# Kernel optimization log

Hardware: AMD Instinct MI355X
Metric: run time of the kernel (lower is better)

The kernel has to match this reference:

```python
import jax, jax.numpy as jnp
import numpy as np

NUM_COMPONENTS = 8   # component ids 1..8 present; 0 = background (excluded, as in ids[ids>0])
SMOOTH = 1e-5


def setup_inputs() -> dict:
    key = jax.random.key(0)
    k1, k2, k3 = jax.random.split(key, 3)
    B, H, W, D = 2, 160, 160, 160
    y_pred = jax.random.normal(k1, (B, 2, H, W, D), dtype=jnp.float32)
    y = jax.random.randint(k2, (B, 1, H, W, D), 0, 2).astype(jnp.int64)
    components = jax.random.randint(k3, (B, H, W, D), 0, NUM_COMPONENTS + 1).astype(jnp.int64)
    return {"y_pred": y_pred, "y": y, "components": components}


def _soft_dice_loss(inter, psum, tsum):
    # metric(masked_pred, masked_true, mask) = 1 - 2*sum(p*t)/(sum(p)+sum(t)), smoothed
    return 1.0 - (2.0 * inter + SMOOTH) / (psum + tsum + SMOOTH)


def reference(y_pred, y, components):
    # activation: softmax over channel dim 1 (binary logits)
    probs = jax.nn.softmax(y_pred, axis=1)                       # [B,2,H,W,D]
    # one-hot encode int labels -> [B,2,H,W,D] float
    true = jax.nn.one_hot(y[:, 0], y_pred.shape[1], axis=1, dtype=probs.dtype)
    B = probs.shape[0]
    V = components.shape[1] * components.shape[2] * components.shape[3]
    comp = components.reshape(B, V)
    # per-voxel channel-summed quantities (mask-multiply then reduce == segment reduce)
    pp = (probs * true).sum(axis=1).reshape(B, V)                # sum_c p*t
    sp = probs.sum(axis=1).reshape(B, V)                         # sum_c p
    st = true.sum(axis=1).reshape(B, V)                          # sum_c t
    cnt = jnp.ones((B, V), dtype=probs.dtype)

    def seg(d):
        return jax.vmap(lambda dd, cc: jax.ops.segment_sum(dd, cc, num_segments=NUM_COMPONENTS + 1))(d, comp)

    inter, psum, tsum, counts = seg(pp), seg(sp), seg(st), seg(cnt)
    # drop background (component id 0), as torch loops only over ids > 0
    inter, psum, tsum, counts = inter[:, 1:], psum[:, 1:], tsum[:, 1:], counts[:, 1:]
    dice = _soft_dice_loss(inter, psum, tsum)                    # [B, K]
    present = (counts > 0).astype(dice.dtype)                    # only ids in torch.unique
    per_sample = (dice * present).sum(axis=1) / jnp.maximum(present.sum(axis=1), 1.0)
    return per_sample.mean()
```

## Files before the change

kernel.cpp:

```cpp
#include <hip/hip_runtime.h>

#define NB 2
#define NCK 8
#define NVAL (NCK * 2)
#define NBINS (NB * NVAL)
#define SMOOTHF 1e-5f

#define TROW 18

__global__ __launch_bounds__(256) void cc_accum(
        const float* __restrict__ y_pred,
        const int* __restrict__ y,
        const int* __restrict__ comp,
        float* __restrict__ partial,
        int V4, int BPB, int nblk) {
    __shared__ __align__(8) float sacc[256 * TROW + 16 * 16];
    float* redbuf = &sacc[256 * TROW];

    float2* mybins = (float2*)&sacc[threadIdx.x * TROW];
    #pragma unroll
    for (int i = 0; i < 9; ++i) mybins[i] = make_float2(0.0f, 0.0f);

    const int b   = (blockIdx.x >= BPB) ? 1 : 0;
    const int blk = blockIdx.x - b * BPB;
    const int stride = BPB * 256;

    const float* p0 = y_pred + (size_t)b * 2 * ((size_t)V4 * 4);
    const float* p1 = p0 + (size_t)V4 * 4;
    const int4* yq = (const int4*)y    + (size_t)b * V4;
    const int4* cq = (const int4*)comp + (size_t)b * V4;

    for (int v = blk * 256 + threadIdx.x; v < V4; v += stride) {
        const float4 a0 = ((const float4*)p0)[v];
        const float4 a1 = ((const float4*)p1)[v];
        const int4 t = yq[v];
        const int4 c = cq[v];

        {
            const float d = a0.x - a1.x;
            const float p = 1.0f / (1.0f + __expf(t.x ? d : -d));
            float2 s = mybins[c.x]; s.x += p; s.y += 1.0f; mybins[c.x] = s;
        }
        {
            const float d = a0.y - a1.y;
            const float p = 1.0f / (1.0f + __expf(t.y ? d : -d));
            float2 s = mybins[c.y]; s.x += p; s.y += 1.0f; mybins[c.y] = s;
        }
        {
            const float d = a0.z - a1.z;
            const float p = 1.0f / (1.0f + __expf(t.z ? d : -d));
            float2 s = mybins[c.z]; s.x += p; s.y += 1.0f; mybins[c.z] = s;
        }
        {
            const float d = a0.w - a1.w;
            const float p = 1.0f / (1.0f + __expf(t.w ? d : -d));
            float2 s = mybins[c.w]; s.x += p; s.y += 1.0f; mybins[c.w] = s;
        }
    }
    __syncthreads();

    {
        const int v = threadIdx.x & 15, g = threadIdx.x >> 4;
        const int off = ((v >> 1) + 1) * 2 + (v & 1);
        float s = 0.0f;
        #pragma unroll
        for (int k = 0; k < 16; ++k)
            s += sacc[(g * 16 + k) * TROW + off];
        redbuf[v * 16 + g] = s;
    }
    __syncthreads();
    if (threadIdx.x < NVAL) {
        float s = 0.0f;
        #pragma unroll
        for (int g = 0; g < 16; ++g) s += redbuf[threadIdx.x * 16 + g];
        partial[(size_t)(b * NVAL + threadIdx.x) * nblk + blockIdx.x] = s;
    }
}

__global__ __launch_bounds__(256) void cc_reduce(
        const float* __restrict__ partial, float* __restrict__ fin,
        int half, int nblk) {
    const int bin = blockIdx.x;
    const int b = (bin >= NVAL) ? 1 : 0;
    const int c0 = b * half;
    float s = 0.0f;
    for (int i = threadIdx.x; i < half; i += 256)
        s += partial[(size_t)bin * nblk + c0 + i];
    #pragma unroll
    for (int off = 32; off; off >>= 1) s += __shfl_xor(s, off);
    __shared__ float w4[4];
    if ((threadIdx.x & 63) == 0) w4[threadIdx.x >> 6] = s;
    __syncthreads();
    if (threadIdx.x == 0) fin[bin] = w4[0] + w4[1] + w4[2] + w4[3];
}

__global__ void cc_final(const float* __restrict__ fin, float* __restrict__ out) {
    float total = 0.0f;
    for (int b = 0; b < NB; ++b) {
        float dsum = 0.0f, pc = 0.0f;
        for (int j = 0; j < NCK; ++j) {
            const float inter = fin[b * NVAL + 2 * j];
            const float cnt   = fin[b * NVAL + 2 * j + 1];
            if (cnt > 0.0f) {
                dsum += 1.0f - (2.0f * inter + SMOOTHF) / (2.0f * cnt + SMOOTHF);
                pc += 1.0f;
            }
        }
        total += dsum / fmaxf(pc, 1.0f);
    }
    out[0] = total / (float)NB;
}

extern "C" void kernel_launch(void* const* d_in, const int* in_sizes, int n_in,
                              void* d_out, int out_size, void* d_ws, size_t ws_size,
                              hipStream_t stream) {
    const float* y_pred = (const float*)d_in[0];
    const int*   y      = (const int*)d_in[1];
    const int*   comp   = (const int*)d_in[2];
    float* out = (float*)d_out;
    float* ws  = (float*)d_ws;

    const int nvox = in_sizes[1];
    const int V    = nvox / NB;
    const int V4   = V / 4;

    int BPB = 1024;
    int cap_rows = (int)((ws_size / sizeof(float) - NBINS) / NBINS);
    if (2 * BPB > cap_rows) BPB = cap_rows / 2;
    if (BPB > V4) BPB = V4;
    if (BPB < 1) BPB = 1;
    const int nblk = 2 * BPB;

    float* fin = ws + (size_t)NBINS * nblk;

    cc_accum<<<dim3(nblk), dim3(256), 0, stream>>>(y_pred, y, comp, ws, V4, BPB, nblk);
    cc_reduce<<<dim3(NBINS), dim3(256), 0, stream>>>(ws, fin, BPB, nblk);
    cc_final<<<dim3(1), dim3(1), 0, stream>>>(fin, out);
}
```

Baseline: 31.18 us.

## Fuse reduce and final kernels into one block, pad shared rows for banks

Partials are now stored block-major (32 slots per block, zeros in the other batch's slots), so one 1024-thread block can sum them with float4 loads and compute the dice loss in the same kernel. This replaces two launches (cc_reduce and cc_final) with one. Shared-memory rows also get a 2-float pad on alternate half-groups of 16 threads to cut bank conflicts in the per-thread histograms. The trade-off is that a single block reads all partials serially and twice as many partial values are written.

```diff
diff --git a/kernel.cpp b/kernel.cpp
--- a/kernel.cpp
+++ b/kernel.cpp
@@ -3,21 +3,22 @@
 #define NB 2
 #define NCK 8
 #define NVAL (NCK * 2)
-#define NBINS (NB * NVAL)
+#define NSL 32
 #define SMOOTHF 1e-5f
 
 #define TROW 18
+#define RBASE(t) ((t) * TROW + ((((t) >> 4) & 1) << 1))
 
 __global__ __launch_bounds__(256) void cc_accum(
         const float* __restrict__ y_pred,
         const int* __restrict__ y,
         const int* __restrict__ comp,
         float* __restrict__ partial,
-        int V4, int BPB, int nblk) {
-    __shared__ __align__(8) float sacc[256 * TROW + 16 * 16];
-    float* redbuf = &sacc[256 * TROW];
+        int V4, int BPB) {
+    __shared__ __align__(8) float sacc[256 * TROW + 4 + 16 * 16];
+    float* redbuf = &sacc[256 * TROW + 4];
 
-    float2* mybins = (float2*)&sacc[threadIdx.x * TROW];
+    float2* mybins = (float2*)&sacc[RBASE(threadIdx.x)];
     #pragma unroll
     for (int i = 0; i < 9; ++i) mybins[i] = make_float2(0.0f, 0.0f);
 
@@ -60,55 +61,89 @@
     __syncthreads();
 
     {
-        const int v = threadIdx.x & 15, g = threadIdx.x >> 4;
-        const int off = ((v >> 1) + 1) * 2 + (v & 1);
+        const int vv = threadIdx.x & 15, g = threadIdx.x >> 4;
+        const int off = ((vv >> 1) + 1) * 2 + (vv & 1);
         float s = 0.0f;
         #pragma unroll
         for (int k = 0; k < 16; ++k)
-            s += sacc[(g * 16 + k) * TROW + off];
-        redbuf[v * 16 + g] = s;
+            s += sacc[RBASE(g * 16 + k) + off];
+        redbuf[vv * 16 + g] = s;
     }
     __syncthreads();
-    if (threadIdx.x < NVAL) {
+    if (threadIdx.x < NSL) {
+        const int j = threadIdx.x, jb = j >> 4, jv = j & 15;
         float s = 0.0f;
-        #pragma unroll
-        for (int g = 0; g < 16; ++g) s += redbuf[threadIdx.x * 16 + g];
-        partial[(size_t)(b * NVAL + threadIdx.x) * nblk + blockIdx.x] = s;
+        if (jb == b) {
+            #pragma unroll
+            for (int g = 0; g < 16; ++g) s += redbuf[jv * 16 + g];
+        }
+        partial[(size_t)blockIdx.x * NSL + j] = s;
     }
 }
 
-__global__ __launch_bounds__(256) void cc_reduce(
-        const float* __restrict__ partial, float* __restrict__ fin,
-        int half, int nblk) {
-    const int bin = blockIdx.x;
-    const int b = (bin >= NVAL) ? 1 : 0;
-    const int c0 = b * half;
-    float s = 0.0f;
-    for (int i = threadIdx.x; i < half; i += 256)
-        s += partial[(size_t)bin * nblk + c0 + i];
-    #pragma unroll
-    for (int off = 32; off; off >>= 1) s += __shfl_xor(s, off);
-    __shared__ float w4[4];
-    if ((threadIdx.x & 63) == 0) w4[threadIdx.x >> 6] = s;
+__global__ __launch_bounds__(1024) void cc_finish(
+        const float* __restrict__ partial, float* __restrict__ out, int nblk) {
+    const int tid = threadIdx.x;
+    const float4* p4 = (const float4*)partial;
+    const int nf = nblk * (NSL / 4);
+
+    float4 a = make_float4(0.f, 0.f, 0.f, 0.f);
+    for (int f = tid; f < nf; f += 1024) {
+        const float4 v = p4[f];
+        a.x += v.x; a.y += v.y; a.z += v.z; a.w += v.w;
+    }
+
+    __shared__ float4 red[1024];
+    red[tid] = a;
     __syncthreads();
-    if (threadIdx.x == 0) fin[bin] = w4[0] + w4[1] + w4[2] + w4[3];
-}
-
-__global__ void cc_final(const float* __restrict__ fin, float* __restrict__ out) {
-    float total = 0.0f;
-    for (int b = 0; b < NB; ++b) {
-        float dsum = 0.0f, pc = 0.0f;
-        for (int j = 0; j < NCK; ++j) {
-            const float inter = fin[b * NVAL + 2 * j];
-            const float cnt   = fin[b * NVAL + 2 * j + 1];
-            if (cnt > 0.0f) {
-                dsum += 1.0f - (2.0f * inter + SMOOTHF) / (2.0f * cnt + SMOOTHF);
-                pc += 1.0f;
+    if (tid < 256) {
+        float4 r = red[tid];
+        const float4 s1 = red[tid + 256], s2 = red[tid + 512], s3 = red[tid + 768];
+        r.x += s1.x + s2.x + s3.x;
+        r.y += s1.y + s2.y + s3.y;
+        r.z += s1.z + s2.z + s3.z;
+        r.w += s1.w + s2.w + s3.w;
+        red[tid] = r;
+    }
+    __syncthreads();
+    if (tid < 64) {
+        float4 r = red[tid];
+        const float4 s1 = red[tid + 64], s2 = red[tid + 128], s3 = red[tid + 192];
+        r.x += s1.x + s2.x + s3.x;
+        r.y += s1.y + s2.y + s3.y;
+        r.z += s1.z + s2.z + s3.z;
+        r.w += s1.w + s2.w + s3.w;
+        red[tid] = r;
+    }
+    __syncthreads();
+    __shared__ float fin[NSL];
+    if (tid < NSL) {
+        const int grp = tid >> 2, k = tid & 3;
+        float s = 0.0f;
+        #pragma unroll
+        for (int g = 0; g < 8; ++g) {
+            const float4 r = red[g * 8 + grp];
+            s += (k == 0) ? r.x : (k == 1) ? r.y : (k == 2) ? r.z : r.w;
+        }
+        fin[tid] = s;
+    }
+    __syncthreads();
+    if (tid == 0) {
+        float total = 0.0f;
+        for (int b = 0; b < NB; ++b) {
+            float dsum = 0.0f, pc = 0.0f;
+            for (int j = 0; j < NCK; ++j) {
+                const float inter = fin[b * NVAL + 2 * j];
+                const float cnt   = fin[b * NVAL + 2 * j + 1];
+                if (cnt > 0.0f) {
+                    dsum += 1.0f - (2.0f * inter + SMOOTHF) / (2.0f * cnt + SMOOTHF);
+                    pc += 1.0f;
+                }
             }
+            total += dsum / fmaxf(pc, 1.0f);
         }
-        total += dsum / fmaxf(pc, 1.0f);
+        out[0] = total / (float)NB;
     }
-    out[0] = total / (float)NB;
 }
 
 extern "C" void kernel_launch(void* const* d_in, const int* in_sizes, int n_in,
@@ -125,15 +160,12 @@
     const int V4   = V / 4;
 
     int BPB = 1024;
-    int cap_rows = (int)((ws_size / sizeof(float) - NBINS) / NBINS);
+    int cap_rows = (int)(ws_size / (NSL * sizeof(float)));
     if (2 * BPB > cap_rows) BPB = cap_rows / 2;
     if (BPB > V4) BPB = V4;
     if (BPB < 1) BPB = 1;
     const int nblk = 2 * BPB;
 
-    float* fin = ws + (size_t)NBINS * nblk;
-
-    cc_accum<<<dim3(nblk), dim3(256), 0, stream>>>(y_pred, y, comp, ws, V4, BPB, nblk);
-    cc_reduce<<<dim3(NBINS), dim3(256), 0, stream>>>(ws, fin, BPB, nblk);
-    cc_final<<<dim3(1), dim3(1), 0, stream>>>(fin, out);
+    cc_accum<<<dim3(nblk), dim3(256), 0, stream>>>(y_pred, y, comp, ws, V4, BPB);
+    cc_finish<<<dim3(1), dim3(1024), 0, stream>>>(ws, out, nblk);
 }
```

After: 33.65 us. +7.9%, slower.

## Transpose shared-memory bins and fold final dice step into reduce via ticket

Applied to the files above, without the earlier changes.

The per-thread histogram bins move from a row-per-thread layout with stride 18 to a bin-major [9][256] float2 layout, so the data-dependent read-modify-writes hit distinct LDS banks across threads. The final single-thread kernel is removed. The last cc_reduce block, chosen with an atomic ticket counter, now computes the dice loss, which saves one kernel launch. In exchange the code adds atomics and fences, and the ticket is reset inside the first kernel.

```diff
diff --git a/kernel.cpp b/kernel.cpp
--- a/kernel.cpp
+++ b/kernel.cpp
@@ -6,20 +6,19 @@
 #define NBINS (NB * NVAL)
 #define SMOOTHF 1e-5f
 
-#define TROW 18
-
 __global__ __launch_bounds__(256) void cc_accum(
         const float* __restrict__ y_pred,
         const int* __restrict__ y,
         const int* __restrict__ comp,
         float* __restrict__ partial,
+        int* __restrict__ ticket,
         int V4, int BPB, int nblk) {
-    __shared__ __align__(8) float sacc[256 * TROW + 16 * 16];
-    float* redbuf = &sacc[256 * TROW];
+    __shared__ __align__(8) float2 bins[9][256];
+    __shared__ float redbuf[16 * 17];
 
-    float2* mybins = (float2*)&sacc[threadIdx.x * TROW];
     #pragma unroll
-    for (int i = 0; i < 9; ++i) mybins[i] = make_float2(0.0f, 0.0f);
+    for (int i = 0; i < 9; ++i) bins[i][threadIdx.x] = make_float2(0.0f, 0.0f);
+    if (blockIdx.x == 0 && threadIdx.x == 0) *ticket = 0;
 
     const int b   = (blockIdx.x >= BPB) ? 1 : 0;
     const int blk = blockIdx.x - b * BPB;
@@ -39,46 +38,49 @@
         {
             const float d = a0.x - a1.x;
             const float p = 1.0f / (1.0f + __expf(t.x ? d : -d));
-            float2 s = mybins[c.x]; s.x += p; s.y += 1.0f; mybins[c.x] = s;
+            float2 s = bins[c.x][threadIdx.x]; s.x += p; s.y += 1.0f; bins[c.x][threadIdx.x] = s;
         }
         {
             const float d = a0.y - a1.y;
             const float p = 1.0f / (1.0f + __expf(t.y ? d : -d));
-            float2 s = mybins[c.y]; s.x += p; s.y += 1.0f; mybins[c.y] = s;
+            float2 s = bins[c.y][threadIdx.x]; s.x += p; s.y += 1.0f; bins[c.y][threadIdx.x] = s;
         }
         {
             const float d = a0.z - a1.z;
             const float p = 1.0f / (1.0f + __expf(t.z ? d : -d));
-            float2 s = mybins[c.z]; s.x += p; s.y += 1.0f; mybins[c.z] = s;
+            float2 s = bins[c.z][threadIdx.x]; s.x += p; s.y += 1.0f; bins[c.z][threadIdx.x] = s;
         }
         {
             const float d = a0.w - a1.w;
             const float p = 1.0f / (1.0f + __expf(t.w ? d : -d));
-            float2 s = mybins[c.w]; s.x += p; s.y += 1.0f; mybins[c.w] = s;
+            float2 s = bins[c.w][threadIdx.x]; s.x += p; s.y += 1.0f; bins[c.w][threadIdx.x] = s;
         }
     }
     __syncthreads();
 
     {
-        const int v = threadIdx.x & 15, g = threadIdx.x >> 4;
-        const int off = ((v >> 1) + 1) * 2 + (v & 1);
+        const int vv = threadIdx.x >> 4, q = threadIdx.x & 15;
+        const int c  = (vv >> 1) + 1, part = vv & 1;
+        const float* base = (const float*)&bins[c][0];
         float s = 0.0f;
         #pragma unroll
         for (int k = 0; k < 16; ++k)
-            s += sacc[(g * 16 + k) * TROW + off];
-        redbuf[v * 16 + g] = s;
+            s += base[(q + 16 * k) * 2 + part];
+        redbuf[vv * 17 + q] = s;
     }
     __syncthreads();
     if (threadIdx.x < NVAL) {
+        const int j = threadIdx.x;
         float s = 0.0f;
         #pragma unroll
-        for (int g = 0; g < 16; ++g) s += redbuf[threadIdx.x * 16 + g];
-        partial[(size_t)(b * NVAL + threadIdx.x) * nblk + blockIdx.x] = s;
+        for (int q = 0; q < 16; ++q) s += redbuf[j * 17 + q];
+        partial[(size_t)(b * NVAL + j) * nblk + blockIdx.x] = s;
     }
 }
 
 __global__ __launch_bounds__(256) void cc_reduce(
         const float* __restrict__ partial, float* __restrict__ fin,
+        int* __restrict__ ticket, float* __restrict__ out,
         int half, int nblk) {
     const int bin = blockIdx.x;
     const int b = (bin >= NVAL) ? 1 : 0;
@@ -91,24 +93,33 @@
     __shared__ float w4[4];
     if ((threadIdx.x & 63) == 0) w4[threadIdx.x >> 6] = s;
     __syncthreads();
-    if (threadIdx.x == 0) fin[bin] = w4[0] + w4[1] + w4[2] + w4[3];
-}
-
-__global__ void cc_final(const float* __restrict__ fin, float* __restrict__ out) {
-    float total = 0.0f;
-    for (int b = 0; b < NB; ++b) {
-        float dsum = 0.0f, pc = 0.0f;
-        for (int j = 0; j < NCK; ++j) {
-            const float inter = fin[b * NVAL + 2 * j];
-            const float cnt   = fin[b * NVAL + 2 * j + 1];
-            if (cnt > 0.0f) {
-                dsum += 1.0f - (2.0f * inter + SMOOTHF) / (2.0f * cnt + SMOOTHF);
-                pc += 1.0f;
+    if (threadIdx.x == 0) {
+        const float tot = w4[0] + w4[1] + w4[2] + w4[3];
+        atomicExch(&fin[bin], tot);
+        __threadfence();
+        const int old = atomicAdd(ticket, 1);
+        if (old == NBINS - 1) {
+            __threadfence();
+            float v[NBINS];
+            #pragma unroll
+            for (int i = 0; i < NBINS; ++i)
+                v[i] = atomicAdd(&fin[i], 0.0f);
+            float total = 0.0f;
+            for (int bb = 0; bb < NB; ++bb) {
+                float dsum = 0.0f, pc = 0.0f;
+                for (int j = 0; j < NCK; ++j) {
+                    const float inter = v[bb * NVAL + 2 * j];
+                    const float cnt   = v[bb * NVAL + 2 * j + 1];
+                    if (cnt > 0.0f) {
+                        dsum += 1.0f - (2.0f * inter + SMOOTHF) / (2.0f * cnt + SMOOTHF);
+                        pc += 1.0f;
+                    }
+                }
+                total += dsum / fmaxf(pc, 1.0f);
             }
+            out[0] = total / (float)NB;
         }
-        total += dsum / fmaxf(pc, 1.0f);
     }
-    out[0] = total / (float)NB;
 }
 
 extern "C" void kernel_launch(void* const* d_in, const int* in_sizes, int n_in,
@@ -125,15 +136,15 @@
     const int V4   = V / 4;
 
     int BPB = 1024;
-    int cap_rows = (int)((ws_size / sizeof(float) - NBINS) / NBINS);
+    int cap_rows = (int)((ws_size / sizeof(float) - NBINS - 4) / NBINS);
     if (2 * BPB > cap_rows) BPB = cap_rows / 2;
     if (BPB > V4) BPB = V4;
     if (BPB < 1) BPB = 1;
     const int nblk = 2 * BPB;
 
-    float* fin = ws + (size_t)NBINS * nblk;
+    float* fin    = ws + (size_t)NBINS * nblk;
+    int*   ticket = (int*)(fin + NBINS);
 
-    cc_accum<<<dim3(nblk), dim3(256), 0, stream>>>(y_pred, y, comp, ws, V4, BPB, nblk);
-    cc_reduce<<<dim3(NBINS), dim3(256), 0, stream>>>(ws, fin, BPB, nblk);
-    cc_final<<<dim3(1), dim3(1), 0, stream>>>(fin, out);
+    cc_accum<<<dim3(nblk), dim3(256), 0, stream>>>(y_pred, y, comp, ws, ticket, V4, BPB, nblk);
+    cc_reduce<<<dim3(NBINS), dim3(256), 0, stream>>>(ws, fin, ticket, out, BPB, nblk);
 }
```

Result: slower. 42.03 us (+34.8%).
